# Performance work log

Measured on AMD Instinct MI355X. Metric: run time of the kernel, lower is better.

The kernel has to match this reference:

```python
import jax, jax.numpy as jnp
import numpy as np

SIZE_DICT = 1024  # K
DIM_DICT = 256    # D


def setup_inputs() -> dict:
    key = jax.random.key(0)
    k1, k2, k3 = jax.random.split(key, 3)
    z = jax.random.normal(k1, (64, 1024, DIM_DICT), dtype=jnp.float32)
    codebook = jax.random.normal(k2, (SIZE_DICT, DIM_DICT), dtype=jnp.float32)
    codebook_weight = jax.random.normal(k3, (SIZE_DICT,), dtype=jnp.float32)
    return {
        "z_from_encoder": z,
        "codebook": codebook,
        "codebook_weight": codebook_weight,
        "flg_train": 0,
    }


def reference(z_from_encoder, codebook, codebook_weight, flg_train):
    z = z_from_encoder
    z_flat = z.reshape(-1, DIM_DICT)  # [N, D]
    # Pairwise squared distances: ||z||^2 + ||c||^2 - 2 z.c  -> [N, K]
    cost = (
        jnp.sum(z_flat ** 2, axis=1, keepdims=True)
        + jnp.sum(codebook ** 2, axis=1)
        - 2.0 * jnp.matmul(z_flat, codebook.T)
    )
    idx = jnp.argmin(cost, axis=1)  # [N]
    # one-hot scatter + matmul with codebook == gather of codebook rows
    z_q = codebook[idx].reshape(z.shape)
    # straight-through estimator
    z_q = z + jax.lax.stop_gradient(z_q - z)
    # loss is 0.0 in eval (flg_train False)
    loss = jnp.float32(0.0)
    # perplexity from mean one-hot encodings
    n = z_flat.shape[0]
    counts = jnp.zeros((SIZE_DICT,), dtype=jnp.float32).at[idx].add(1.0)
    e_mean = counts / n
    perplexity = jnp.exp(-jnp.sum(e_mean * jnp.log(e_mean + 1e-10)))
    return z_q, loss, perplexity
```

## Files before the change

### kernel.cpp

```cpp
#include <hip/hip_runtime.h>
#include <hip/hip_bf16.h>
#include <stdint.h>


typedef float  v4f __attribute__((ext_vector_type(4)));
typedef _Float16 v8h __attribute__((ext_vector_type(8)));
typedef _Float16 v4h __attribute__((ext_vector_type(4)));

#define N_ROWS 65536
#define N_DICT 1024
#define DIMS   256
#define MARGIN 4e-3f

__device__ __forceinline__ void gl_lds16(const void* g, void* l) {
  __builtin_amdgcn_global_load_lds(
      (const __attribute__((address_space(1))) unsigned int*)g,
      (__attribute__((address_space(3))) unsigned int*)l,
      16, 0, 0);
}

__global__ void k_prep(const float* __restrict__ cb, _Float16* __restrict__ swz_h,
                       _Float16* __restrict__ swz_l, float* __restrict__ cnA,
                       double* __restrict__ cnD,
                       unsigned* __restrict__ hist, unsigned* __restrict__ counters) {
  const int b = blockIdx.x, t = threadIdx.x;
  if (b == 0) {
    for (int i = t; i < N_DICT; i += 256) hist[i] = 0u;
    if (t == 0) { counters[0] = 0u; counters[1] = 0u; }
  }
  const int gid = b * 256 + t;
  const int col = gid >> 6;
  const int k0  = (gid & 63) * 4;
  v4f v = ((const v4f*)cb)[gid];
  v4h h, l;
  #pragma unroll
  for (int j = 0; j < 4; ++j) {
    h[j] = (_Float16)v[j];
    float r = v[j] - (float)h[j];
    l[j] = (_Float16)r;
  }
  const int c = col >> 6, t4 = (col >> 4) & 3, l15 = col & 15;
  const int kk = k0 >> 5, q = (k0 >> 3) & 3, j0 = k0 & 7;
  const size_t off = (size_t)(((c * 8 + kk) * 4 + t4) * 512 + (q * 16 + l15) * 8 + j0);
  *(v4h*)(swz_h + off) = h;
  *(v4h*)(swz_l + off) = l;
  const int lane = t & 63, w = t >> 6;
  const int row = b * 4 + w;
  v4f u = ((const v4f*)cb)[row * 64 + lane];
  double s = (double)u[0]*u[0] + (double)u[1]*u[1]
           + (double)u[2]*u[2] + (double)u[3]*u[3];
  #pragma unroll
  for (int d = 1; d < 64; d <<= 1) s += __shfl_xor(s, d);
  if (lane == 0) { cnA[row] = (float)s; cnD[row] = s; }
}

__launch_bounds__(256, 2)
__global__ void k_main(const float* __restrict__ z, const float* __restrict__ cb,
                       const _Float16* __restrict__ swz_h, const _Float16* __restrict__ swz_l,
                       const float* __restrict__ cnA,
                       float* __restrict__ outz,
                       unsigned* __restrict__ out_idx,
                       unsigned long long* __restrict__ list1,
                       unsigned* __restrict__ list2,
                       unsigned* __restrict__ hist,
                       unsigned* __restrict__ counters) {
  __shared__ __align__(16) char lds[2][32768];
  __shared__ float lds_cn[N_DICT];
  const int t = threadIdx.x, lane = t & 63, w = t >> 6;
  const int l15 = lane & 15, q = lane >> 4;
  const int waverow = (blockIdx.x * 4 + w) * 32;

  for (int i = t; i < N_DICT; i += 256) lds_cn[i] = cnA[i];

  v8h ah[2][8], al[2][8];
  #pragma unroll
  for (int m = 0; m < 2; ++m) {
    const float* zp = z + (size_t)(waverow + m * 16 + l15) * DIMS + q * 8;
    #pragma unroll
    for (int kk = 0; kk < 8; ++kk) {
      v4f f0 = *(const v4f*)(zp + kk * 32);
      v4f f1 = *(const v4f*)(zp + kk * 32 + 4);
      v8h hh, ll;
      #pragma unroll
      for (int j = 0; j < 4; ++j) {
        hh[j] = (_Float16)f0[j];
        float r = f0[j] - (float)hh[j];
        ll[j] = (_Float16)r;
        hh[4 + j] = (_Float16)f1[j];
        r = f1[j] - (float)hh[4 + j];
        ll[4 + j] = (_Float16)r;
      }
      ah[m][kk] = hh; al[m][kk] = ll;
    }
  }

  const int s0 = w * 8;
  const char* gsrc_base = (const char*)(s0 >= 16 ? swz_l : swz_h);

  float m1[8], m2[8], m3[8]; int c1[8], c2[8];
  #pragma unroll
  for (int s = 0; s < 8; ++s) {
    m1[s] = 1e30f; m2[s] = 1e30f; m3[s] = 1e30f; c1[s] = 0; c2[s] = 0;
  }

  #pragma unroll
  for (int i = 0; i < 8; ++i) {
    const int s = s0 + i, kk = (s >> 1) & 7, u = s & 1;
    const char* gb = gsrc_base + (size_t)(kk * 4096 + u * 1024 + lane * 16);
    gl_lds16(gb, &lds[0][s * 1024]);
  }
  __syncthreads();

  for (int cc = 0; cc < 32; ++cc) {
    if (cc + 1 < 32) {
      const int n = cc + 1, c = n >> 1, half = n & 1;
      char* nbuf = lds[n & 1];
      #pragma unroll
      for (int i = 0; i < 8; ++i) {
        const int s = s0 + i, kk = (s >> 1) & 7, u = s & 1;
        const char* gb = gsrc_base +
            (size_t)(c * 32768 + kk * 4096 + (2 * half + u) * 1024 + lane * 16);
        gl_lds16(gb, nbuf + s * 1024);
      }
    }

    const char* buf = lds[cc & 1];
    const int c = cc >> 1, half = cc & 1;
    const int n0 = c * 64 + half * 32;
    float cn[2]; int colv[2];
    #pragma unroll
    for (int u = 0; u < 2; ++u) {
      colv[u] = n0 + u * 16 + l15;
      cn[u] = lds_cn[colv[u]];
    }
    v4f acc[2][2];
    #pragma unroll
    for (int m = 0; m < 2; ++m)
      #pragma unroll
      for (int u = 0; u < 2; ++u) acc[m][u] = (v4f){0.f, 0.f, 0.f, 0.f};

    #pragma unroll
    for (int kk = 0; kk < 8; ++kk) {
      v8h b_h[2], b_l[2];
      #pragma unroll
      for (int u = 0; u < 2; ++u)
        b_h[u] = *(const v8h*)(buf + (kk * 2 + u) * 1024 + lane * 16);
      #pragma unroll
      for (int u = 0; u < 2; ++u)
        b_l[u] = *(const v8h*)(buf + 16384 + (kk * 2 + u) * 1024 + lane * 16);
      #pragma unroll
      for (int m = 0; m < 2; ++m) {
        #pragma unroll
        for (int u = 0; u < 2; ++u)
          acc[m][u] = __builtin_amdgcn_mfma_f32_16x16x32_f16(ah[m][kk], b_h[u], acc[m][u], 0, 0, 0);
        #pragma unroll
        for (int u = 0; u < 2; ++u)
          acc[m][u] = __builtin_amdgcn_mfma_f32_16x16x32_f16(al[m][kk], b_h[u], acc[m][u], 0, 0, 0);
        #pragma unroll
        for (int u = 0; u < 2; ++u)
          acc[m][u] = __builtin_amdgcn_mfma_f32_16x16x32_f16(ah[m][kk], b_l[u], acc[m][u], 0, 0, 0);
      }
    }
    #pragma unroll
    for (int m = 0; m < 2; ++m)
      #pragma unroll
      for (int u = 0; u < 2; ++u)
        #pragma unroll
        for (int r = 0; r < 4; ++r) {
          float cost = fmaf(acc[m][u][r], -2.0f, cn[u]);
          const int s = m * 4 + r;
          bool lt1 = cost < m1[s];
          bool lt2 = cost < m2[s];
          bool lt3 = cost < m3[s];
          m3[s] = lt2 ? m2[s] : (lt3 ? cost : m3[s]);
          m2[s] = lt1 ? m1[s] : (lt2 ? cost : m2[s]);
          c2[s] = lt1 ? c1[s] : (lt2 ? colv[u] : c2[s]);
          m1[s] = lt1 ? cost : m1[s];
          c1[s] = lt1 ? colv[u] : c1[s];
        }
    __syncthreads();
  }

  #pragma unroll
  for (int d = 1; d < 16; d <<= 1) {
    #pragma unroll
    for (int s = 0; s < 8; ++s) {
      float om1 = __shfl_xor(m1[s], d);
      float om2 = __shfl_xor(m2[s], d);
      float om3 = __shfl_xor(m3[s], d);
      int   oc1 = __shfl_xor(c1[s], d);
      int   oc2 = __shfl_xor(c2[s], d);
      bool take = (om1 < m1[s]) || (om1 == m1[s] && oc1 < c1[s]);
      float w1 = take ? om1 : m1[s];  int wc1 = take ? oc1 : c1[s];
      float w2 = take ? om2 : m2[s];  int wc2 = take ? oc2 : c2[s];
      float w3 = take ? om3 : m3[s];
      float l1 = take ? m1[s] : om1;  int lc1 = take ? c1[s] : oc1;
      float l2 = take ? m2[s] : om2;
      bool t2 = (l1 < w2) || (l1 == w2 && lc1 < wc2);
      m1[s] = w1; c1[s] = wc1;
      m2[s] = t2 ? l1 : w2;
      c2[s] = t2 ? lc1 : wc2;
      m3[s] = t2 ? fminf(w2, l2) : fminf(w3, l1);
    }
  }
  #pragma unroll
  for (int s = 0; s < 8; ++s) {
    const int m = s >> 2, r = s & 3;
    const int row = waverow + m * 16 + q * 4 + r;
    const unsigned id = (unsigned)c1[s];
    if (l15 == s) {
      out_idx[row] = id;
      atomicAdd(hist + id, 1u);
      if (m3[s] - m1[s] < MARGIN) {
        unsigned pos = atomicAdd(&counters[1], 1u);
        list2[pos] = (unsigned)row;
      } else if (m2[s] - m1[s] < MARGIN) {
        unsigned pos = atomicAdd(&counters[0], 1u);
        list1[pos] = (unsigned long long)row
                   | ((unsigned long long)id << 20)
                   | ((unsigned long long)(unsigned)c2[s] << 40);
      }
    }
    const float* src = cb + (size_t)id * DIMS + l15 * 16;
    float* dst = outz + (size_t)row * DIMS + l15 * 16;
    v4f t0 = *(const v4f*)(src + 0);
    v4f t1 = *(const v4f*)(src + 4);
    v4f t2v = *(const v4f*)(src + 8);
    v4f t3 = *(const v4f*)(src + 12);
    *(v4f*)(dst + 0) = t0;  *(v4f*)(dst + 4) = t1;
    *(v4f*)(dst + 8) = t2v; *(v4f*)(dst + 12) = t3;
  }
}

__global__ void k_resolve(const float* __restrict__ z, const float* __restrict__ cb,
                          const double* __restrict__ cnD,
                          const unsigned long long* __restrict__ list1,
                          const unsigned* __restrict__ list2,
                          const unsigned* __restrict__ counters,
                          unsigned* __restrict__ out_idx,
                          unsigned* __restrict__ hist,
                          float* __restrict__ outz) {
  const int t = threadIdx.x, lane = t & 63, w = t >> 6;
  if (blockIdx.x < 2048) {
    const unsigned count = counters[0];
    if (count == 0) return;
    const unsigned gw = blockIdx.x * 4 + w;
    const int half = lane >> 5, l5 = lane & 31;
    for (unsigned g = gw; g < count; g += 8192) {
      const unsigned long long e = list1[g];
      const unsigned row = (unsigned)(e & 0xFFFFFu);
      const int c1 = (int)((e >> 20) & 0x3FFu);
      const int c2 = (int)((e >> 40) & 0x3FFu);
      const int col = half ? c2 : c1;
      const float* cp = cb + (size_t)col * DIMS + l5 * 8;
      const float* zr = z + (size_t)row * DIMS + l5 * 8;
      v4f z0 = *(const v4f*)zr,  z1 = *(const v4f*)(zr + 4);
      v4f cc0 = *(const v4f*)cp, cc1 = *(const v4f*)(cp + 4);
      double a = (double)z0[0] * (double)cc0[0];
      a = fma((double)z0[1], (double)cc0[1], a);
      a = fma((double)z0[2], (double)cc0[2], a);
      a = fma((double)z0[3], (double)cc0[3], a);
      a = fma((double)z1[0], (double)cc1[0], a);
      a = fma((double)z1[1], (double)cc1[1], a);
      a = fma((double)z1[2], (double)cc1[2], a);
      a = fma((double)z1[3], (double)cc1[3], a);
      #pragma unroll
      for (int d = 1; d < 32; d <<= 1) a += __shfl_xor(a, d);
      double cost = cnD[col] - 2.0 * a;
      double oc = __shfl_xor(cost, 32);
      int win = 0;
      if (lane == 0) {
        bool take = (oc < cost) || (oc == cost && c2 < c1);
        win = take ? c2 : c1;
      }
      win = __shfl(win, 0);
      if (win != c1) {
        if (lane == 0) {
          out_idx[row] = (unsigned)win;
          atomicAdd(hist + win, 1u);
          atomicAdd(hist + c1, 0xFFFFFFFFu);
        }
        if (lane < 16) {
          const float* src = cb + (size_t)win * DIMS + lane * 16;
          float* dst = outz + (size_t)row * DIMS + lane * 16;
          v4f t0 = *(const v4f*)(src + 0);
          v4f t1 = *(const v4f*)(src + 4);
          v4f t2v = *(const v4f*)(src + 8);
          v4f t3 = *(const v4f*)(src + 12);
          *(v4f*)(dst + 0) = t0;  *(v4f*)(dst + 4) = t1;
          *(v4f*)(dst + 8) = t2v; *(v4f*)(dst + 12) = t3;
        }
      }
    }
  } else {
    const unsigned count = counters[1];
    if (count == 0) return;
    __shared__ double sc[4];
    __shared__ int scc[4];
    __shared__ int s_win;
    __shared__ unsigned s_old;
    for (unsigned g = blockIdx.x - 2048; g < count; g += 1024) {
      const unsigned row = list2[g];
      const float* zr = z + (size_t)row * DIMS;
      double best = 1e300; int bc = 1 << 30;
      for (int ci = w * 4; ci < w * 4 + 4; ++ci) {
        const int col = ci * 64 + lane;
        const float* cp = cb + (size_t)col * DIMS;
        double a0 = 0, a1 = 0, a2 = 0, a3 = 0, a4 = 0, a5 = 0, a6 = 0, a7 = 0;
        #pragma unroll 8
        for (int k = 0; k < DIMS; k += 8) {
          v4f z0 = *(const v4f*)(zr + k);
          v4f z1 = *(const v4f*)(zr + k + 4);
          v4f cc0 = *(const v4f*)(cp + k);
          v4f cc1 = *(const v4f*)(cp + k + 4);
          a0 = fma((double)z0[0], (double)cc0[0], a0);
          a1 = fma((double)z0[1], (double)cc0[1], a1);
          a2 = fma((double)z0[2], (double)cc0[2], a2);
          a3 = fma((double)z0[3], (double)cc0[3], a3);
          a4 = fma((double)z1[0], (double)cc1[0], a4);
          a5 = fma((double)z1[1], (double)cc1[1], a5);
          a6 = fma((double)z1[2], (double)cc1[2], a6);
          a7 = fma((double)z1[3], (double)cc1[3], a7);
        }
        double cost = cnD[col]
                    - 2.0 * (((a0 + a1) + (a2 + a3)) + ((a4 + a5) + (a6 + a7)));
        if (cost < best || (cost == best && col < bc)) { best = cost; bc = col; }
      }
      #pragma unroll
      for (int d = 1; d < 64; d <<= 1) {
        double ob = __shfl_xor(best, d);
        int    oc = __shfl_xor(bc, d);
        if (ob < best || (ob == best && oc < bc)) { best = ob; bc = oc; }
      }
      if (lane == 0) { sc[w] = best; scc[w] = bc; }
      __syncthreads();
      if (t == 0) {
        double b = sc[0]; int c = scc[0];
        #pragma unroll
        for (int i = 1; i < 4; ++i)
          if (sc[i] < b || (sc[i] == b && scc[i] < c)) { b = sc[i]; c = scc[i]; }
        unsigned old = out_idx[row];
        s_win = c; s_old = old;
        if ((unsigned)c != old) {
          out_idx[row] = (unsigned)c;
          atomicAdd(hist + c, 1u);
          atomicAdd(hist + old, 0xFFFFFFFFu);
        }
      }
      __syncthreads();
      if ((unsigned)s_win != s_old && t < 16) {
        const float* src = cb + (size_t)s_win * DIMS + t * 16;
        float* dst = outz + (size_t)row * DIMS + t * 16;
        v4f t0 = *(const v4f*)(src + 0);
        v4f t1 = *(const v4f*)(src + 4);
        v4f t2v = *(const v4f*)(src + 8);
        v4f t3 = *(const v4f*)(src + 12);
        *(v4f*)(dst + 0) = t0;  *(v4f*)(dst + 4) = t1;
        *(v4f*)(dst + 8) = t2v; *(v4f*)(dst + 12) = t3;
      }
      __syncthreads();
    }
  }
}

__global__ void k_stats(const unsigned* __restrict__ hist, float* __restrict__ out) {
  const int t = threadIdx.x;
  float s = 0.f;
  for (int i = t; i < N_DICT; i += 256) {
    float p = (float)hist[i] * (1.0f / (float)N_ROWS);
    s += p * logf(p + 1e-10f);
  }
  #pragma unroll
  for (int d = 1; d < 64; d <<= 1) s += __shfl_xor(s, d);
  __shared__ float ls[4];
  if ((t & 63) == 0) ls[t >> 6] = s;
  __syncthreads();
  if (t == 0) {
    float tot = ls[0] + ls[1] + ls[2] + ls[3];
    out[16777216] = 0.0f;
    out[16777217] = expf(-tot);
  }
}

extern "C" void kernel_launch(void* const* d_in, const int* in_sizes, int n_in,
                              void* d_out, int out_size, void* d_ws, size_t ws_size,
                              hipStream_t stream) {
  const float* z  = (const float*)d_in[0];
  const float* cb = (const float*)d_in[1];
  float* out = (float*)d_out;
  char* ws = (char*)d_ws;
  _Float16* swz_h            = (_Float16*)ws;
  _Float16* swz_l            = (_Float16*)(ws + 524288);
  float*    cnA              = (float*)(ws + 1048576);
  double*   cnD              = (double*)(ws + 1052672);
  unsigned* idx              = (unsigned*)(ws + 1060864);
  unsigned long long* list1  = (unsigned long long*)(ws + 1323008);
  unsigned* list2            = (unsigned*)(ws + 1847296);
  unsigned* hist             = (unsigned*)(ws + 2109440);
  unsigned* counters         = (unsigned*)(ws + 2113536);

  k_prep   <<<256,  256, 0, stream>>>(cb, swz_h, swz_l, cnA, cnD, hist, counters);
  k_main   <<<512,  256, 0, stream>>>(z, cb, swz_h, swz_l, cnA, out, idx, list1, list2, hist, counters);
  k_resolve<<<3072, 256, 0, stream>>>(z, cb, cnD, list1, list2, counters, idx, hist, out);
  k_stats  <<<1,    256, 0, stream>>>(hist, out);
}
```

Baseline: 241.7 us.

## Fuse prep, main, resolve and stats into one cooperative kernel with grid syncs

Replaces the four separate launches with a single cooperative kernel that uses grid.sync between the codebook prep, the distance/argmin pass, the near-tie resolve pass and the gather/perplexity pass. The z loads and fp16 split are moved before the first grid sync so they overlap with codebook preparation. The aim is to remove launch gaps and tail effects between kernels. In exchange, the resolve and gather phases now run on only 512 blocks instead of the original larger grids, and grid-wide barriers add their own cost. The old four-kernel path stays as a fallback if the cooperative launch fails.

```diff
diff --git a/kernel.cpp b/kernel.cpp
--- a/kernel.cpp
+++ b/kernel.cpp
@@ -1,6 +1,9 @@
 #include <hip/hip_runtime.h>
+#include <hip/hip_cooperative_groups.h>
 #include <hip/hip_bf16.h>
 #include <stdint.h>
+
+namespace cg = cooperative_groups;
 
 
 typedef float  v4f __attribute__((ext_vector_type(4)));
@@ -17,6 +20,326 @@
       (const __attribute__((address_space(1))) unsigned int*)g,
       (__attribute__((address_space(3))) unsigned int*)l,
       16, 0, 0);
+}
+
+__launch_bounds__(256, 2)
+__global__ void k_fused(const float* __restrict__ z, const float* __restrict__ cb,
+                        _Float16* __restrict__ swz_h, _Float16* __restrict__ swz_l,
+                        float* __restrict__ cnA, double* __restrict__ cnD,
+                        float* __restrict__ outz, unsigned* __restrict__ out_idx,
+                        unsigned long long* __restrict__ list1,
+                        unsigned* __restrict__ list2,
+                        unsigned* __restrict__ hist, unsigned* __restrict__ counters) {
+  cg::grid_group grid = cg::this_grid();
+  __shared__ __align__(16) char lds[2][32768];
+  __shared__ float lds_cn[N_DICT];
+  __shared__ double sc[4];
+  __shared__ int scc[4];
+  __shared__ float ls[4];
+
+  const int t = threadIdx.x, lane = t & 63, w = t >> 6;
+  const int l15 = lane & 15, q = lane >> 4;
+  const int bid = blockIdx.x;
+  const int waverow = (bid * 4 + w) * 32;
+
+  if (bid < 256) {
+    if (bid == 0) {
+      for (int i = t; i < N_DICT; i += 256) hist[i] = 0u;
+      if (t == 0) { counters[0] = 0u; counters[1] = 0u; }
+    }
+    const int gid = bid * 256 + t;
+    const int col = gid >> 6;
+    const int k0  = (gid & 63) * 4;
+    v4f v = ((const v4f*)cb)[gid];
+    v4h h, l;
+    #pragma unroll
+    for (int j = 0; j < 4; ++j) {
+      h[j] = (_Float16)v[j];
+      float r = v[j] - (float)h[j];
+      l[j] = (_Float16)r;
+    }
+    const int c = col >> 6, t4 = (col >> 4) & 3, cl = col & 15;
+    const int kk = k0 >> 5, qq = (k0 >> 3) & 3, j0 = k0 & 7;
+    const size_t off = (size_t)(((c * 8 + kk) * 4 + t4) * 512 + (qq * 16 + cl) * 8 + j0);
+    *(v4h*)(swz_h + off) = h;
+    *(v4h*)(swz_l + off) = l;
+    const int crow = bid * 4 + w;
+    v4f u = ((const v4f*)cb)[crow * 64 + lane];
+    double s = (double)u[0]*u[0] + (double)u[1]*u[1]
+             + (double)u[2]*u[2] + (double)u[3]*u[3];
+    #pragma unroll
+    for (int d = 1; d < 64; d <<= 1) s += __shfl_xor(s, d);
+    if (lane == 0) { cnA[crow] = (float)s; cnD[crow] = s; }
+  }
+
+  v8h ah[2][8], al[2][8];
+  #pragma unroll
+  for (int m = 0; m < 2; ++m) {
+    const float* zp = z + (size_t)(waverow + m * 16 + l15) * DIMS + q * 8;
+    #pragma unroll
+    for (int kk = 0; kk < 8; ++kk) {
+      v4f f0 = *(const v4f*)(zp + kk * 32);
+      v4f f1 = *(const v4f*)(zp + kk * 32 + 4);
+      v8h hh, ll;
+      #pragma unroll
+      for (int j = 0; j < 4; ++j) {
+        hh[j] = (_Float16)f0[j];
+        float r = f0[j] - (float)hh[j];
+        ll[j] = (_Float16)r;
+        hh[4 + j] = (_Float16)f1[j];
+        r = f1[j] - (float)hh[4 + j];
+        ll[4 + j] = (_Float16)r;
+      }
+      ah[m][kk] = hh; al[m][kk] = ll;
+    }
+  }
+
+  grid.sync();
+
+  for (int i = t; i < N_DICT; i += 256) lds_cn[i] = cnA[i];
+
+  const int s0 = w * 8;
+  const char* gsrc_base = (const char*)(s0 >= 16 ? swz_l : swz_h);
+
+  float m1[8], m2[8], m3[8]; int c1[8], c2[8];
+  #pragma unroll
+  for (int s = 0; s < 8; ++s) {
+    m1[s] = 1e30f; m2[s] = 1e30f; m3[s] = 1e30f; c1[s] = 0; c2[s] = 0;
+  }
+
+  #pragma unroll
+  for (int i = 0; i < 8; ++i) {
+    const int s = s0 + i, kk = (s >> 1) & 7, u = s & 1;
+    const char* gb = gsrc_base + (size_t)(kk * 4096 + u * 1024 + lane * 16);
+    gl_lds16(gb, &lds[0][s * 1024]);
+  }
+  __syncthreads();
+
+  for (int cc = 0; cc < 32; ++cc) {
+    if (cc + 1 < 32) {
+      const int n = cc + 1, c = n >> 1, half = n & 1;
+      char* nbuf = lds[n & 1];
+      #pragma unroll
+      for (int i = 0; i < 8; ++i) {
+        const int s = s0 + i, kk = (s >> 1) & 7, u = s & 1;
+        const char* gb = gsrc_base +
+            (size_t)(c * 32768 + kk * 4096 + (2 * half + u) * 1024 + lane * 16);
+        gl_lds16(gb, nbuf + s * 1024);
+      }
+    }
+
+    const char* buf = lds[cc & 1];
+    const int c = cc >> 1, half = cc & 1;
+    const int n0 = c * 64 + half * 32;
+    float cn[2]; int colv[2];
+    #pragma unroll
+    for (int u = 0; u < 2; ++u) {
+      colv[u] = n0 + u * 16 + l15;
+      cn[u] = lds_cn[colv[u]];
+    }
+    v4f acc[2][2];
+    #pragma unroll
+    for (int m = 0; m < 2; ++m)
+      #pragma unroll
+      for (int u = 0; u < 2; ++u) acc[m][u] = (v4f){0.f, 0.f, 0.f, 0.f};
+
+    #pragma unroll
+    for (int kk = 0; kk < 8; ++kk) {
+      v8h b_h[2], b_l[2];
+      #pragma unroll
+      for (int u = 0; u < 2; ++u)
+        b_h[u] = *(const v8h*)(buf + (kk * 2 + u) * 1024 + lane * 16);
+      #pragma unroll
+      for (int u = 0; u < 2; ++u)
+        b_l[u] = *(const v8h*)(buf + 16384 + (kk * 2 + u) * 1024 + lane * 16);
+      #pragma unroll
+      for (int m = 0; m < 2; ++m) {
+        #pragma unroll
+        for (int u = 0; u < 2; ++u)
+          acc[m][u] = __builtin_amdgcn_mfma_f32_16x16x32_f16(ah[m][kk], b_h[u], acc[m][u], 0, 0, 0);
+        #pragma unroll
+        for (int u = 0; u < 2; ++u)
+          acc[m][u] = __builtin_amdgcn_mfma_f32_16x16x32_f16(al[m][kk], b_h[u], acc[m][u], 0, 0, 0);
+        #pragma unroll
+        for (int u = 0; u < 2; ++u)
+          acc[m][u] = __builtin_amdgcn_mfma_f32_16x16x32_f16(ah[m][kk], b_l[u], acc[m][u], 0, 0, 0);
+      }
+    }
+    #pragma unroll
+    for (int m = 0; m < 2; ++m)
+      #pragma unroll
+      for (int u = 0; u < 2; ++u)
+        #pragma unroll
+        for (int r = 0; r < 4; ++r) {
+          float cost = fmaf(acc[m][u][r], -2.0f, cn[u]);
+          const int s = m * 4 + r;
+          bool lt1 = cost < m1[s];
+          bool lt2 = cost < m2[s];
+          bool lt3 = cost < m3[s];
+          m3[s] = lt2 ? m2[s] : (lt3 ? cost : m3[s]);
+          m2[s] = lt1 ? m1[s] : (lt2 ? cost : m2[s]);
+          c2[s] = lt1 ? c1[s] : (lt2 ? colv[u] : c2[s]);
+          m1[s] = lt1 ? cost : m1[s];
+          c1[s] = lt1 ? colv[u] : c1[s];
+        }
+    __syncthreads();
+  }
+
+  #pragma unroll
+  for (int d = 1; d < 16; d <<= 1) {
+    #pragma unroll
+    for (int s = 0; s < 8; ++s) {
+      float om1 = __shfl_xor(m1[s], d);
+      float om2 = __shfl_xor(m2[s], d);
+      float om3 = __shfl_xor(m3[s], d);
+      int   oc1 = __shfl_xor(c1[s], d);
+      int   oc2 = __shfl_xor(c2[s], d);
+      bool take = (om1 < m1[s]) || (om1 == m1[s] && oc1 < c1[s]);
+      float w1 = take ? om1 : m1[s];  int wc1 = take ? oc1 : c1[s];
+      float w2 = take ? om2 : m2[s];  int wc2 = take ? oc2 : c2[s];
+      float w3 = take ? om3 : m3[s];
+      float l1 = take ? m1[s] : om1;  int lc1 = take ? c1[s] : oc1;
+      float l2 = take ? m2[s] : om2;
+      bool t2 = (l1 < w2) || (l1 == w2 && lc1 < wc2);
+      m1[s] = w1; c1[s] = wc1;
+      m2[s] = t2 ? l1 : w2;
+      c2[s] = t2 ? lc1 : wc2;
+      m3[s] = t2 ? fminf(w2, l2) : fminf(w3, l1);
+    }
+  }
+  if (l15 < 8) {
+    const int s = l15, m = s >> 2, r = s & 3;
+    const int row = waverow + m * 16 + q * 4 + r;
+    const unsigned id = (unsigned)c1[s];
+    out_idx[row] = id;
+    atomicAdd(hist + id, 1u);
+    if (m3[s] - m1[s] < MARGIN) {
+      unsigned pos = atomicAdd(&counters[1], 1u);
+      list2[pos] = (unsigned)row;
+    } else if (m2[s] - m1[s] < MARGIN) {
+      unsigned pos = atomicAdd(&counters[0], 1u);
+      list1[pos] = (unsigned long long)row
+                 | ((unsigned long long)id << 20)
+                 | ((unsigned long long)(unsigned)c2[s] << 40);
+    }
+  }
+
+  grid.sync();
+
+  {
+    const unsigned count = counters[0];
+    const unsigned gw = bid * 4 + w;
+    const int half = lane >> 5, l5 = lane & 31;
+    for (unsigned g = gw; g < count; g += 2048) {
+      const unsigned long long e = list1[g];
+      const unsigned row = (unsigned)(e & 0xFFFFFu);
+      const int cc1 = (int)((e >> 20) & 0x3FFu);
+      const int cc2 = (int)((e >> 40) & 0x3FFu);
+      const int col = half ? cc2 : cc1;
+      const float* cp = cb + (size_t)col * DIMS + l5 * 8;
+      const float* zr = z + (size_t)row * DIMS + l5 * 8;
+      v4f z0 = *(const v4f*)zr,  z1 = *(const v4f*)(zr + 4);
+      v4f cc0 = *(const v4f*)cp, ccv = *(const v4f*)(cp + 4);
+      double a = (double)z0[0] * (double)cc0[0];
+      a = fma((double)z0[1], (double)cc0[1], a);
+      a = fma((double)z0[2], (double)cc0[2], a);
+      a = fma((double)z0[3], (double)cc0[3], a);
+      a = fma((double)z1[0], (double)ccv[0], a);
+      a = fma((double)z1[1], (double)ccv[1], a);
+      a = fma((double)z1[2], (double)ccv[2], a);
+      a = fma((double)z1[3], (double)ccv[3], a);
+      #pragma unroll
+      for (int d = 1; d < 32; d <<= 1) a += __shfl_xor(a, d);
+      double cost = cnD[col] - 2.0 * a;
+      double oc = __shfl_xor(cost, 32);
+      if (lane == 0) {
+        bool take = (oc < cost) || (oc == cost && cc2 < cc1);
+        if (take) {
+          out_idx[row] = (unsigned)cc2;
+          atomicAdd(hist + cc2, 1u);
+          atomicAdd(hist + cc1, 0xFFFFFFFFu);
+        }
+      }
+    }
+    const unsigned count2 = counters[1];
+    for (unsigned g = bid; g < count2; g += 512) {
+      const unsigned row = list2[g];
+      const float* zr = z + (size_t)row * DIMS;
+      double best = 1e300; int bc = 1 << 30;
+      for (int ci = w * 4; ci < w * 4 + 4; ++ci) {
+        const int col = ci * 64 + lane;
+        const float* cp = cb + (size_t)col * DIMS;
+        double a0 = 0, a1 = 0, a2 = 0, a3 = 0, a4 = 0, a5 = 0, a6 = 0, a7 = 0;
+        #pragma unroll 8
+        for (int k = 0; k < DIMS; k += 8) {
+          v4f z0 = *(const v4f*)(zr + k);
+          v4f z1 = *(const v4f*)(zr + k + 4);
+          v4f cc0 = *(const v4f*)(cp + k);
+          v4f cc1v = *(const v4f*)(cp + k + 4);
+          a0 = fma((double)z0[0], (double)cc0[0], a0);
+          a1 = fma((double)z0[1], (double)cc0[1], a1);
+          a2 = fma((double)z0[2], (double)cc0[2], a2);
+          a3 = fma((double)z0[3], (double)cc0[3], a3);
+          a4 = fma((double)z1[0], (double)cc1v[0], a4);
+          a5 = fma((double)z1[1], (double)cc1v[1], a5);
+          a6 = fma((double)z1[2], (double)cc1v[2], a6);
+          a7 = fma((double)z1[3], (double)cc1v[3], a7);
+        }
+        double cost = cnD[col]
+                    - 2.0 * (((a0 + a1) + (a2 + a3)) + ((a4 + a5) + (a6 + a7)));
+        if (cost < best || (cost == best && col < bc)) { best = cost; bc = col; }
+      }
+      #pragma unroll
+      for (int d = 1; d < 64; d <<= 1) {
+        double ob = __shfl_xor(best, d);
+        int    oc = __shfl_xor(bc, d);
+        if (ob < best || (ob == best && oc < bc)) { best = ob; bc = oc; }
+      }
+      if (lane == 0) { sc[w] = best; scc[w] = bc; }
+      __syncthreads();
+      if (t == 0) {
+        double b = sc[0]; int c = scc[0];
+        #pragma unroll
+        for (int i = 1; i < 4; ++i)
+          if (sc[i] < b || (sc[i] == b && scc[i] < c)) { b = sc[i]; c = scc[i]; }
+        unsigned old = out_idx[row];
+        if ((unsigned)c != old) {
+          out_idx[row] = (unsigned)c;
+          atomicAdd(hist + c, 1u);
+          atomicAdd(hist + old, 0xFFFFFFFFu);
+        }
+      }
+      __syncthreads();
+    }
+  }
+
+  grid.sync();
+
+  {
+    const int gbase = (bid * 4 + w) * 32;
+    for (int r = 0; r < 32; ++r) {
+      const int row = gbase + r;
+      const unsigned id = out_idx[row];
+      v4f v = *(const v4f*)(cb + (size_t)id * DIMS + lane * 4);
+      *(v4f*)(outz + (size_t)row * DIMS + lane * 4) = v;
+    }
+  }
+  if (bid == 0) {
+    float s = 0.f;
+    for (int i = t; i < N_DICT; i += 256) {
+      float p = (float)hist[i] * (1.0f / (float)N_ROWS);
+      s += p * logf(p + 1e-10f);
+    }
+    #pragma unroll
+    for (int d = 1; d < 64; d <<= 1) s += __shfl_xor(s, d);
+    if ((t & 63) == 0) ls[t >> 6] = s;
+    __syncthreads();
+    if (t == 0) {
+      float tot = ls[0] + ls[1] + ls[2] + ls[3];
+      outz[16777216] = 0.0f;
+      outz[16777217] = expf(-tot);
+    }
+  }
 }
 
 __global__ void k_prep(const float* __restrict__ cb, _Float16* __restrict__ swz_h,
@@ -69,9 +392,7 @@
   const int t = threadIdx.x, lane = t & 63, w = t >> 6;
   const int l15 = lane & 15, q = lane >> 4;
   const int waverow = (blockIdx.x * 4 + w) * 32;
-
   for (int i = t; i < N_DICT; i += 256) lds_cn[i] = cnA[i];
-
   v8h ah[2][8], al[2][8];
   #pragma unroll
   for (int m = 0; m < 2; ++m) {
@@ -93,24 +414,19 @@
       ah[m][kk] = hh; al[m][kk] = ll;
     }
   }
-
   const int s0 = w * 8;
   const char* gsrc_base = (const char*)(s0 >= 16 ? swz_l : swz_h);
-
   float m1[8], m2[8], m3[8]; int c1[8], c2[8];
   #pragma unroll
   for (int s = 0; s < 8; ++s) {
     m1[s] = 1e30f; m2[s] = 1e30f; m3[s] = 1e30f; c1[s] = 0; c2[s] = 0;
   }
-
   #pragma unroll
   for (int i = 0; i < 8; ++i) {
     const int s = s0 + i, kk = (s >> 1) & 7, u = s & 1;
-    const char* gb = gsrc_base + (size_t)(kk * 4096 + u * 1024 + lane * 16);
-    gl_lds16(gb, &lds[0][s * 1024]);
+    gl_lds16(gsrc_base + (size_t)(kk * 4096 + u * 1024 + lane * 16), &lds[0][s * 1024]);
   }
   __syncthreads();
-
   for (int cc = 0; cc < 32; ++cc) {
     if (cc + 1 < 32) {
       const int n = cc + 1, c = n >> 1, half = n & 1;
@@ -118,36 +434,28 @@
       #pragma unroll
       for (int i = 0; i < 8; ++i) {
         const int s = s0 + i, kk = (s >> 1) & 7, u = s & 1;
-        const char* gb = gsrc_base +
-            (size_t)(c * 32768 + kk * 4096 + (2 * half + u) * 1024 + lane * 16);
-        gl_lds16(gb, nbuf + s * 1024);
-      }
-    }
-
+        gl_lds16(gsrc_base + (size_t)(c * 32768 + kk * 4096 + (2 * half + u) * 1024 + lane * 16),
+                 nbuf + s * 1024);
+      }
+    }
     const char* buf = lds[cc & 1];
     const int c = cc >> 1, half = cc & 1;
     const int n0 = c * 64 + half * 32;
     float cn[2]; int colv[2];
     #pragma unroll
-    for (int u = 0; u < 2; ++u) {
-      colv[u] = n0 + u * 16 + l15;
-      cn[u] = lds_cn[colv[u]];
-    }
+    for (int u = 0; u < 2; ++u) { colv[u] = n0 + u * 16 + l15; cn[u] = lds_cn[colv[u]]; }
     v4f acc[2][2];
     #pragma unroll
     for (int m = 0; m < 2; ++m)
       #pragma unroll
       for (int u = 0; u < 2; ++u) acc[m][u] = (v4f){0.f, 0.f, 0.f, 0.f};
-
     #pragma unroll
     for (int kk = 0; kk < 8; ++kk) {
       v8h b_h[2], b_l[2];
       #pragma unroll
-      for (int u = 0; u < 2; ++u)
-        b_h[u] = *(const v8h*)(buf + (kk * 2 + u) * 1024 + lane * 16);
-      #pragma unroll
-      for (int u = 0; u < 2; ++u)
-        b_l[u] = *(const v8h*)(buf + 16384 + (kk * 2 + u) * 1024 + lane * 16);
+      for (int u = 0; u < 2; ++u) b_h[u] = *(const v8h*)(buf + (kk * 2 + u) * 1024 + lane * 16);
+      #pragma unroll
+      for (int u = 0; u < 2; ++u) b_l[u] = *(const v8h*)(buf + 16384 + (kk * 2 + u) * 1024 + lane * 16);
       #pragma unroll
       for (int m = 0; m < 2; ++m) {
         #pragma unroll
@@ -180,7 +488,6 @@
         }
     __syncthreads();
   }
-
   #pragma unroll
   for (int d = 1; d < 16; d <<= 1) {
     #pragma unroll
@@ -399,8 +706,15 @@
   unsigned* hist             = (unsigned*)(ws + 2109440);
   unsigned* counters         = (unsigned*)(ws + 2113536);
 
-  k_prep   <<<256,  256, 0, stream>>>(cb, swz_h, swz_l, cnA, cnD, hist, counters);
-  k_main   <<<512,  256, 0, stream>>>(z, cb, swz_h, swz_l, cnA, out, idx, list1, list2, hist, counters);
-  k_resolve<<<3072, 256, 0, stream>>>(z, cb, cnD, list1, list2, counters, idx, hist, out);
-  k_stats  <<<1,    256, 0, stream>>>(hist, out);
+  void* args[] = {(void*)&z, (void*)&cb, (void*)&swz_h, (void*)&swz_l,
+                  (void*)&cnA, (void*)&cnD, (void*)&out, (void*)&idx,
+                  (void*)&list1, (void*)&list2, (void*)&hist, (void*)&counters};
+  hipError_t err = hipLaunchCooperativeKernel((const void*)k_fused,
+                                              dim3(512), dim3(256), args, 0, stream);
+  if (err != hipSuccess) {
+    k_prep   <<<256,  256, 0, stream>>>(cb, swz_h, swz_l, cnA, cnD, hist, counters);
+    k_main   <<<512,  256, 0, stream>>>(z, cb, swz_h, swz_l, cnA, out, idx, list1, list2, hist, counters);
+    k_resolve<<<3072, 256, 0, stream>>>(z, cb, cnD, list1, list2, counters, idx, hist, out);
+    k_stats  <<<1,    256, 0, stream>>>(hist, out);
+  }
 }
```

Measured after the change: 406.6 us. +68.2%, slower.
